# Optimization experiments

Hardware: AMD Instinct MI355X
Metric: run time of the kernel (lower is better)

## Reference

```python
import jax, jax.numpy as jnp
import numpy as np

N_NODES = 100000
N_EDGES = 1600000
IN_DIM = 128
HID = 64
OUT_DIM = 3


def _glorot(key, shape):
    fan_in, fan_out = shape[0], shape[1]
    std = (2.0 / (fan_in + fan_out)) ** 0.5
    return jax.random.normal(key, shape, jnp.float32) * std


def setup_inputs() -> dict:
    key = jax.random.key(0)
    ks = jax.random.split(key, 12)
    x = jax.random.normal(ks[0], (N_NODES, IN_DIM), jnp.float32)
    edge_index = jax.random.randint(ks[1], (2, N_EDGES), 0, N_NODES, dtype=jnp.int32)
    return {
        "x": x,
        "edge_index": edge_index,
        "W1": _glorot(ks[2], (IN_DIM, HID)), "b1": jnp.zeros((HID,), jnp.float32),
        "W2": _glorot(ks[3], (HID, HID)), "b2": jnp.zeros((HID,), jnp.float32),
        "W3": _glorot(ks[4], (HID, HID)), "b3": jnp.zeros((HID,), jnp.float32),
        "W4": _glorot(ks[5], (HID, HID // 2)), "b4": jnp.zeros((HID // 2,), jnp.float32),
        "Wh": _glorot(ks[6], (HID // 2, OUT_DIM)), "bh": jnp.zeros((OUT_DIM,), jnp.float32),
    }


def reference(x, edge_index, W1, b1, W2, b2, W3, b3, W4, b4, Wh, bh):
    n = x.shape[0]
    self_loops = jnp.arange(n, dtype=edge_index.dtype)
    src = jnp.concatenate([edge_index[0], self_loops])  # message sources j
    dst = jnp.concatenate([edge_index[1], self_loops])  # aggregation targets i
    # symmetric GCN normalization with self-loops: deg over targets (unit edge weights)
    deg = jax.ops.segment_sum(jnp.ones_like(dst, jnp.float32), dst, num_segments=n)
    dinv = jnp.where(deg > 0, jax.lax.rsqrt(deg), 0.0)
    norm = dinv[src] * dinv[dst]  # [E+N]

    def gcn(h, W, b):
        h = h @ W  # transform first (PyG GCNConv order)
        agg = jax.ops.segment_sum(h[src] * norm[:, None], dst, num_segments=n)
        return agg + b

    h = jax.nn.relu(gcn(x, W1, b1))   # dropout is identity in eval mode
    h = jax.nn.relu(gcn(h, W2, b2))
    h = jax.nn.relu(gcn(h, W3, b3))
    h = jax.nn.relu(gcn(h, W4, b4))
    return h @ Wh + bh  # [N, 3]
```

## Files before the change

kernel.cpp:

```cpp
#include <hip/hip_runtime.h>
#include <hip/hip_bf16.h>
#include <hip/hip_fp16.h>
#include <cstdint>


#define MAXD 512
#define EB   8192
#define PADSLACK 2048

__device__ __forceinline__ void hist_body(const int* __restrict__ ei,
                                          int* __restrict__ histM, int E, int b) {
    __shared__ int hist[MAXD];
    const int tid = threadIdx.x;
    hist[tid] = 0; hist[tid + 256] = 0;
    __syncthreads();
    const int base = b * EB;
#pragma unroll 2
    for (int it = 0; it < EB / 256; it += 4) {
        int d[4]; bool ok[4];
#pragma unroll
        for (int u = 0; u < 4; ++u) {
            int e = base + (it + u) * 256 + tid;
            ok[u] = e < E;
            d[u] = ok[u] ? ei[E + e] : 0;
        }
#pragma unroll
        for (int u = 0; u < 4; ++u)
            if (ok[u]) atomicAdd(&hist[d[u] >> 8], 1);
    }
    __syncthreads();
    histM[(size_t)b * MAXD + tid] = hist[tid];
    histM[(size_t)b * MAXD + tid + 256] = hist[tid + 256];
}

__global__ __launch_bounds__(256) void scan_digits_k(int* __restrict__ histM,
                                                     int* __restrict__ totals,
                                                     int NBLK) {
    __shared__ int s[256];
    const int t = threadIdx.x, dg = blockIdx.x;
    int v = (t < NBLK) ? histM[(size_t)t * MAXD + dg] : 0;
    s[t] = v;
    __syncthreads();
    for (int off = 1; off < 256; off <<= 1) {
        int x = (t >= off) ? s[t - off] : 0;
        __syncthreads();
        s[t] += x;
        __syncthreads();
    }
    if (t < NBLK) histM[(size_t)t * MAXD + dg] = s[t] - v;
    if (t == 255) totals[dg] = s[255];
}

__global__ __launch_bounds__(512) void scan_base_k(const int* __restrict__ totals,
                                                   int* __restrict__ cb, int ND) {
    __shared__ int s[512];
    const int t = threadIdx.x;
    int v = (t < ND) ? totals[t] : 0;
    s[t] = v;
    __syncthreads();
    for (int off = 1; off < 512; off <<= 1) {
        int x = (t >= off) ? s[t - off] : 0;
        __syncthreads();
        s[t] += x;
        __syncthreads();
    }
    if (t < ND) cb[t] = s[t] - v;
    if (t == 511) cb[ND] = s[511];
}

template <int K, int OUT, bool HALF_OUT>
__device__ __forceinline__ void gemm_body(const float* __restrict__ H,
                                          const float* __restrict__ W,
                                          const float* __restrict__ dinv,
                                          void* __restrict__ Tout, int n, int bx) {
    constexpr int TX  = OUT / 4;
    constexpr int TY  = 256 / TX;
    constexpr int BM  = TY * 4;
    constexpr int BK  = 32;
    constexpr int PAD = 4;

    __shared__ float At[BK][BM + PAD];
    __shared__ float Ws[BK][OUT];

    const int t    = threadIdx.x;
    const int cx   = t % TX;
    const int ry   = t / TX;
    const int row0 = bx * BM;

    float acc[4][4] = {{0.f}};
    const int arow = t >> 3;
    const int af4  = t & 7;

    for (int k0 = 0; k0 < K; k0 += BK) {
#pragma unroll
        for (int p = 0; p < BM / 32; ++p) {
            int r  = arow + p * 32;
            int gr = row0 + r;
            int grc = gr < n ? gr : n - 1;
            float4 v = *reinterpret_cast<const float4*>(
                H + (size_t)grc * K + k0 + af4 * 4);
            At[af4 * 4 + 0][r] = v.x;
            At[af4 * 4 + 1][r] = v.y;
            At[af4 * 4 + 2][r] = v.z;
            At[af4 * 4 + 3][r] = v.w;
        }
#pragma unroll
        for (int p = 0; p < (BK * OUT) / 1024; ++p) {
            int idx = t + p * 256;
            int wk  = idx / (OUT / 4);
            int wf  = idx % (OUT / 4);
            float4 v = *reinterpret_cast<const float4*>(
                W + (size_t)(k0 + wk) * OUT + wf * 4);
            *reinterpret_cast<float4*>(&Ws[wk][wf * 4]) = v;
        }
        __syncthreads();
#pragma unroll
        for (int k = 0; k < BK; ++k) {
            float4 a = *reinterpret_cast<const float4*>(&At[k][ry * 4]);
            float4 w = *reinterpret_cast<const float4*>(&Ws[k][cx * 4]);
            acc[0][0] = fmaf(a.x, w.x, acc[0][0]);
            acc[0][1] = fmaf(a.x, w.y, acc[0][1]);
            acc[0][2] = fmaf(a.x, w.z, acc[0][2]);
            acc[0][3] = fmaf(a.x, w.w, acc[0][3]);
            acc[1][0] = fmaf(a.y, w.x, acc[1][0]);
            acc[1][1] = fmaf(a.y, w.y, acc[1][1]);
            acc[1][2] = fmaf(a.y, w.z, acc[1][2]);
            acc[1][3] = fmaf(a.y, w.w, acc[1][3]);
            acc[2][0] = fmaf(a.z, w.x, acc[2][0]);
            acc[2][1] = fmaf(a.z, w.y, acc[2][1]);
            acc[2][2] = fmaf(a.z, w.z, acc[2][2]);
            acc[2][3] = fmaf(a.z, w.w, acc[2][3]);
            acc[3][0] = fmaf(a.w, w.x, acc[3][0]);
            acc[3][1] = fmaf(a.w, w.y, acc[3][1]);
            acc[3][2] = fmaf(a.w, w.z, acc[3][2]);
            acc[3][3] = fmaf(a.w, w.w, acc[3][3]);
        }
        __syncthreads();
    }
#pragma unroll
    for (int i = 0; i < 4; ++i) {
        int gr = row0 + ry * 4 + i;
        if (gr < n) {
            if constexpr (HALF_OUT) {
                float di = dinv[gr];
                union { ushort4 u; __half h[4]; } pk;
                pk.h[0] = __float2half_rn(acc[i][0] * di);
                pk.h[1] = __float2half_rn(acc[i][1] * di);
                pk.h[2] = __float2half_rn(acc[i][2] * di);
                pk.h[3] = __float2half_rn(acc[i][3] * di);
                *reinterpret_cast<ushort4*>(
                    (__half*)Tout + (size_t)gr * 64 + cx * 4) = pk.u;
            } else {
                float4 v = make_float4(acc[i][0], acc[i][1], acc[i][2], acc[i][3]);
                *reinterpret_cast<float4*>(
                    (float*)Tout + (size_t)gr * OUT + cx * 4) = v;
            }
        }
    }
}

__device__ __forceinline__ void pack_body(const int* __restrict__ ei,
                                          const int* __restrict__ histM,
                                          const int* __restrict__ cb,
                                          int* __restrict__ packed,
                                          int E, int ND, int b) {
    __shared__ int cur[MAXD];
    const int tid = threadIdx.x;
    for (int t = tid; t < ND; t += 256)
        cur[t] = cb[t] + histM[(size_t)b * MAXD + t];
    __syncthreads();
    const int base = b * EB;
    for (int it = 0; it < EB / 256; it += 4) {
        int s[4], d[4]; bool ok[4];
#pragma unroll
        for (int u = 0; u < 4; ++u) {
            int e = base + (it + u) * 256 + tid;
            ok[u] = e < E;
            if (ok[u]) { s[u] = ei[e]; d[u] = ei[E + e]; }
        }
#pragma unroll
        for (int u = 0; u < 4; ++u) {
            if (ok[u]) {
                int pos = atomicAdd(&cur[d[u] >> 8], 1);
                packed[pos] = (s[u] << 8) | (d[u] & 255);
            }
        }
    }
}

__global__ __launch_bounds__(256) void hist_gemm1_k(
    const int* __restrict__ ei, int* __restrict__ histM, int E,
    const float* __restrict__ x, const float* __restrict__ W1,
    float* __restrict__ T1, int n, int NH) {
    const int bx = blockIdx.x;
    if (bx < NH) hist_body(ei, histM, E, bx);
    else         gemm_body<128, 64, false>(x, W1, nullptr, T1, n, bx - NH);
}

__global__ __launch_bounds__(256) void pack_gemm1_k(
    const int* __restrict__ ei, const int* __restrict__ histM,
    const int* __restrict__ cb, int* __restrict__ packed,
    const float* __restrict__ x, const float* __restrict__ W1,
    float* __restrict__ T1, int n, int E, int ND, int NPB, int G1) {
    const int bx = blockIdx.x;
    if (bx < NPB) pack_body(ei, histM, cb, packed, E, ND, bx);
    else          gemm_body<128, 64, false>(x, W1, nullptr, T1, n, G1 + bx - NPB);
}

__global__ __launch_bounds__(256) void bucket_k(const int* __restrict__ packed,
                                                const int* __restrict__ cb,
                                                int* __restrict__ col,
                                                int* __restrict__ rowptr,
                                                int* __restrict__ counts,
                                                float* __restrict__ dinv,
                                                const float* __restrict__ Traw,
                                                __half* __restrict__ Th, int n) {
    __shared__ int   hist[256];
    __shared__ int   pref[256];
    __shared__ int   cur[256];
    __shared__ float dinv_l[256];

    const int tid   = threadIdx.x;
    const int dg    = blockIdx.x;
    const int base  = cb[dg];
    const int m     = cb[dg + 1] - base;
    const int basep = base + dg * PADSLACK;

    hist[tid] = 0;
    __syncthreads();
    for (int k0 = 0; k0 < m; k0 += 1024) {
        int v[4]; bool ok[4];
#pragma unroll
        for (int u = 0; u < 4; ++u) {
            int k = k0 + u * 256 + tid;
            ok[u] = k < m;
            v[u] = ok[u] ? packed[base + k] : 0;
        }
#pragma unroll
        for (int u = 0; u < 4; ++u)
            if (ok[u]) atomicAdd(&hist[v[u] & 255], 1);
    }
    __syncthreads();
    const int deg   = hist[tid];
    const int cnt_p = (deg + 8) & ~7;
    pref[tid] = cnt_p;
    __syncthreads();
    for (int off = 1; off < 256; off <<= 1) {
        int x = (tid >= off) ? pref[tid - off] : 0;
        __syncthreads();
        pref[tid] += x;
        __syncthreads();
    }
    const int rp = basep + pref[tid] - cnt_p;
    const float di = rsqrtf((float)(deg + 1));
    dinv_l[tid] = di;
    cur[tid] = rp + 1;
    const int d = dg * 256 + tid;
    if (d < n) {
        counts[d] = cnt_p;
        dinv[d]   = di;
        rowptr[d] = rp;
        col[rp]   = d;
        for (int k = deg + 1; k < cnt_p; ++k) col[rp + k] = n;
    }
    __syncthreads();
    for (int k0 = 0; k0 < m; k0 += 1024) {
        int v[4]; bool ok[4];
#pragma unroll
        for (int u = 0; u < 4; ++u) {
            int k = k0 + u * 256 + tid;
            ok[u] = k < m;
            v[u] = ok[u] ? packed[base + k] : 0;
        }
#pragma unroll
        for (int u = 0; u < 4; ++u) {
            if (ok[u]) {
                int pos = atomicAdd(&cur[v[u] & 255], 1);
                col[pos] = v[u] >> 8;
            }
        }
    }
    const int r0 = dg * 256;
#pragma unroll 4
    for (int it = 0; it < 16; ++it) {
        int idx = it * 256 + tid;
        int rl  = idx >> 4;
        int r   = r0 + rl;
        if (r < n) {
            float4 v = reinterpret_cast<const float4*>(Traw)[(size_t)r * 16 + (idx & 15)];
            float dd = dinv_l[rl];
            union { ushort4 u; __half h[4]; } pk;
            pk.h[0] = __float2half_rn(v.x * dd);
            pk.h[1] = __float2half_rn(v.y * dd);
            pk.h[2] = __float2half_rn(v.z * dd);
            pk.h[3] = __float2half_rn(v.w * dd);
            reinterpret_cast<ushort4*>(Th)[(size_t)r * 16 + (idx & 15)] = pk.u;
        }
    }
    if (dg == 0 && tid < 16) {
        uint2 z; z.x = 0u; z.y = 0u;
        reinterpret_cast<uint2*>(Th)[(size_t)n * 16 + tid] = z;
    }
}

template <int K, int OUT>
__global__ __launch_bounds__(256) void gemm_h_k(const float* __restrict__ H,
                                                const float* __restrict__ W,
                                                const float* __restrict__ dinv,
                                                __half* __restrict__ T, int n) {
    gemm_body<K, OUT, true>(H, W, dinv, T, n, blockIdx.x);
}

template <int LR, bool FUSE_HEAD>
__global__ __launch_bounds__(256) void agg_k(const __half* __restrict__ T,
                                             const int* __restrict__ rowptr,
                                             const int* __restrict__ counts,
                                             const int* __restrict__ col,
                                             const float* __restrict__ dinv,
                                             const float* __restrict__ bias,
                                             float* __restrict__ O, int n,
                                             const float* __restrict__ Wh,
                                             const float* __restrict__ bh) {
    constexpr int NSW = 64 / LR;
    constexpr int U   = 16 / NSW;
    constexpr int UH  = U / 2;
    const int lane = threadIdx.x & 63;
    const int q    = lane % LR;
    const int sw   = lane / LR;
    const int i = (blockIdx.x * blockDim.x + threadIdx.x) >> 6;
    if (i >= n) return;

    const int start = rowptr[i];
    const int cnt   = counts[i];
    const uint2* __restrict__ T2 = reinterpret_cast<const uint2*>(T);

    float4 acc = make_float4(0.f, 0.f, 0.f, 0.f);
    for (int base = 0; base < cnt; base += 64) {
        const int m = min(64, cnt - base);
        int c_l = col[start + base + lane];
        int jg = 0;
        for (; jg + 16 <= m; jg += 16) {
            int cc[U]; uint2 v[U];
#pragma unroll
            for (int u = 0; u < U; ++u)
                cc[u] = __shfl(c_l, jg + u * NSW + sw, 64);
#pragma unroll
            for (int u = 0; u < U; ++u) v[u] = T2[(size_t)cc[u] * 16 + q];
#pragma unroll
            for (int u = 0; u < U; ++u) {
                const __half2* h2 = reinterpret_cast<const __half2*>(&v[u]);
                float2 f0 = __half22float2(h2[0]);
                float2 f1 = __half22float2(h2[1]);
                acc.x += f0.x; acc.y += f0.y; acc.z += f1.x; acc.w += f1.y;
            }
        }
        if (jg < m) {
            int cc[UH]; uint2 v[UH];
#pragma unroll
            for (int u = 0; u < UH; ++u)
                cc[u] = __shfl(c_l, jg + u * NSW + sw, 64);
#pragma unroll
            for (int u = 0; u < UH; ++u) v[u] = T2[(size_t)cc[u] * 16 + q];
#pragma unroll
            for (int u = 0; u < UH; ++u) {
                const __half2* h2 = reinterpret_cast<const __half2*>(&v[u]);
                float2 f0 = __half22float2(h2[0]);
                float2 f1 = __half22float2(h2[1]);
                acc.x += f0.x; acc.y += f0.y; acc.z += f1.x; acc.w += f1.y;
            }
        }
    }
#pragma unroll
    for (int off = LR; off < 64; off <<= 1) {
        acc.x += __shfl_xor(acc.x, off, 64);
        acc.y += __shfl_xor(acc.y, off, 64);
        acc.z += __shfl_xor(acc.z, off, 64);
        acc.w += __shfl_xor(acc.w, off, 64);
    }
    const float di = dinv[i];
    const float4 b4 = reinterpret_cast<const float4*>(bias)[q];
    float4 h;
    h.x = fmaxf(fmaf(di, acc.x, b4.x), 0.f);
    h.y = fmaxf(fmaf(di, acc.y, b4.y), 0.f);
    h.z = fmaxf(fmaf(di, acc.z, b4.z), 0.f);
    h.w = fmaxf(fmaf(di, acc.w, b4.w), 0.f);
    if constexpr (!FUSE_HEAD) {
        if (sw == 0)
            reinterpret_cast<float4*>(O + (size_t)i * 64)[q] = h;
    } else {
        float p0 = h.x * Wh[(4 * q + 0) * 3 + 0];
        float p1 = h.x * Wh[(4 * q + 0) * 3 + 1];
        float p2 = h.x * Wh[(4 * q + 0) * 3 + 2];
        p0 = fmaf(h.y, Wh[(4 * q + 1) * 3 + 0], p0);
        p1 = fmaf(h.y, Wh[(4 * q + 1) * 3 + 1], p1);
        p2 = fmaf(h.y, Wh[(4 * q + 1) * 3 + 2], p2);
        p0 = fmaf(h.z, Wh[(4 * q + 2) * 3 + 0], p0);
        p1 = fmaf(h.z, Wh[(4 * q + 2) * 3 + 1], p1);
        p2 = fmaf(h.z, Wh[(4 * q + 2) * 3 + 2], p2);
        p0 = fmaf(h.w, Wh[(4 * q + 3) * 3 + 0], p0);
        p1 = fmaf(h.w, Wh[(4 * q + 3) * 3 + 1], p1);
        p2 = fmaf(h.w, Wh[(4 * q + 3) * 3 + 2], p2);
#pragma unroll
        for (int off = 1; off < LR; off <<= 1) {
            p0 += __shfl_xor(p0, off, 64);
            p1 += __shfl_xor(p1, off, 64);
            p2 += __shfl_xor(p2, off, 64);
        }
        if (lane == 0) {
            O[(size_t)i * 3 + 0] = p0 + bh[0];
            O[(size_t)i * 3 + 1] = p1 + bh[1];
            O[(size_t)i * 3 + 2] = p2 + bh[2];
        }
    }
}

extern "C" void kernel_launch(void* const* d_in, const int* in_sizes, int n_in,
                              void* d_out, int out_size, void* d_ws, size_t ws_size,
                              hipStream_t stream) {
    const float* x  = (const float*)d_in[0];
    const int*   ei = (const int*)d_in[1];
    const float* W1 = (const float*)d_in[2];
    const float* b1 = (const float*)d_in[3];
    const float* W2 = (const float*)d_in[4];
    const float* b2 = (const float*)d_in[5];
    const float* W3 = (const float*)d_in[6];
    const float* b3 = (const float*)d_in[7];
    const float* W4 = (const float*)d_in[8];
    const float* b4 = (const float*)d_in[9];
    const float* Wh = (const float*)d_in[10];
    const float* bh = (const float*)d_in[11];
    float* out = (float*)d_out;

    const int n = in_sizes[0] / 128;
    const int E = in_sizes[1] / 2;
    const int ND   = (n + 255) / 256;
    const int NBLK = (E + EB - 1) / EB;

    char* ws = (char*)d_ws;
    auto alloc = [&](size_t bytes) {
        char* p = ws;
        ws += (bytes + 255) & ~(size_t)255;
        return p;
    };
    int*    histM  = (int*)alloc((size_t)NBLK * MAXD * 4);
    int*    totals = (int*)alloc((size_t)MAXD * 4);
    int*    cbA    = (int*)alloc((size_t)(MAXD + 1) * 4);
    int*    packed = (int*)alloc((size_t)E * 4);
    int*    col    = (int*)alloc(((size_t)E + (size_t)ND * PADSLACK + 256) * 4);
    int*    rowptr = (int*)alloc((size_t)n * 4);
    int*    counts = (int*)alloc((size_t)n * 4);
    float*  dinv   = (float*)alloc((size_t)n * 4);
    float*  bufF   = (float*)alloc((size_t)n * 64 * 4);
    __half* bufH   = (__half*)alloc(((size_t)n + 1) * 64 * 2);

    dim3 blk(256);
    const int G  = (n + 63) / 64;
    const int G1 = G / 3;
    const int G2 = G - G1;
    const int agg_blocks = (n + 3) / 4;

    hist_gemm1_k<<<dim3(NBLK + G1), blk, 0, stream>>>(ei, histM, E, x, W1, bufF, n, NBLK);
    scan_digits_k<<<dim3(ND), blk, 0, stream>>>(histM, totals, NBLK);
    scan_base_k<<<dim3(1), dim3(512), 0, stream>>>(totals, cbA, ND);
    pack_gemm1_k<<<dim3(NBLK + G2), blk, 0, stream>>>(ei, histM, cbA, packed,
                                                      x, W1, bufF, n, E, ND, NBLK, G1);
    bucket_k<<<dim3(ND), blk, 0, stream>>>(packed, cbA, col, rowptr, counts,
                                           dinv, bufF, bufH, n);
    agg_k<16, false><<<dim3(agg_blocks), blk, 0, stream>>>(
        bufH, rowptr, counts, col, dinv, b1, bufF, n, nullptr, nullptr);
    gemm_h_k<64, 64><<<dim3(G), blk, 0, stream>>>(bufF, W2, dinv, bufH, n);
    agg_k<16, false><<<dim3(agg_blocks), blk, 0, stream>>>(
        bufH, rowptr, counts, col, dinv, b2, bufF, n, nullptr, nullptr);
    gemm_h_k<64, 64><<<dim3(G), blk, 0, stream>>>(bufF, W3, dinv, bufH, n);
    agg_k<16, false><<<dim3(agg_blocks), blk, 0, stream>>>(
        bufH, rowptr, counts, col, dinv, b3, bufF, n, nullptr, nullptr);
    gemm_h_k<64, 32><<<dim3((n + 127) / 128), blk, 0, stream>>>(bufF, W4, dinv, bufH, n);
    agg_k<8, true><<<dim3(agg_blocks), blk, 0, stream>>>(
        bufH, rowptr, counts, col, dinv, b4, out, n, Wh, bh);
}
```

Baseline: 383.9 us.

## Use fp16 MFMA for hidden GEMMs and store aggregation outputs in fp16

```diff
diff --git a/kernel.cpp b/kernel.cpp
--- a/kernel.cpp
+++ b/kernel.cpp
@@ -7,6 +7,24 @@
 #define MAXD 512
 #define EB   8192
 #define PADSLACK 2048
+
+typedef _Float16 half8v __attribute__((ext_vector_type(8)));
+typedef _Float16 half2v __attribute__((ext_vector_type(2)));
+typedef float    float4v __attribute__((ext_vector_type(4)));
+
+#if defined(__has_builtin)
+#if __has_builtin(__builtin_amdgcn_fdot2)
+#define HAVE_FDOT2 1
+#endif
+#endif
+
+__device__ __forceinline__ float fdot2f(half2v a, half2v b, float c) {
+#ifdef HAVE_FDOT2
+    return __builtin_amdgcn_fdot2(a, b, c, false);
+#else
+    return c + (float)a[0] * (float)b[0] + (float)a[1] * (float)b[1];
+#endif
+}
 
 __device__ __forceinline__ void hist_body(const int* __restrict__ ei,
                                           int* __restrict__ histM, int E, int b) {
@@ -68,11 +86,10 @@
     if (t == 511) cb[ND] = s[511];
 }
 
-template <int K, int OUT, bool HALF_OUT>
+template <int K, int OUT>
 __device__ __forceinline__ void gemm_body(const float* __restrict__ H,
                                           const float* __restrict__ W,
-                                          const float* __restrict__ dinv,
-                                          void* __restrict__ Tout, int n, int bx) {
+                                          float* __restrict__ Tout, int n, int bx) {
     constexpr int TX  = OUT / 4;
     constexpr int TY  = 256 / TX;
     constexpr int BM  = TY * 4;
@@ -141,20 +158,8 @@
     for (int i = 0; i < 4; ++i) {
         int gr = row0 + ry * 4 + i;
         if (gr < n) {
-            if constexpr (HALF_OUT) {
-                float di = dinv[gr];
-                union { ushort4 u; __half h[4]; } pk;
-                pk.h[0] = __float2half_rn(acc[i][0] * di);
-                pk.h[1] = __float2half_rn(acc[i][1] * di);
-                pk.h[2] = __float2half_rn(acc[i][2] * di);
-                pk.h[3] = __float2half_rn(acc[i][3] * di);
-                *reinterpret_cast<ushort4*>(
-                    (__half*)Tout + (size_t)gr * 64 + cx * 4) = pk.u;
-            } else {
-                float4 v = make_float4(acc[i][0], acc[i][1], acc[i][2], acc[i][3]);
-                *reinterpret_cast<float4*>(
-                    (float*)Tout + (size_t)gr * OUT + cx * 4) = v;
-            }
+            float4 v = make_float4(acc[i][0], acc[i][1], acc[i][2], acc[i][3]);
+            *reinterpret_cast<float4*>(Tout + (size_t)gr * OUT + cx * 4) = v;
         }
     }
 }
@@ -194,7 +199,7 @@
     float* __restrict__ T1, int n, int NH) {
     const int bx = blockIdx.x;
     if (bx < NH) hist_body(ei, histM, E, bx);
-    else         gemm_body<128, 64, false>(x, W1, nullptr, T1, n, bx - NH);
+    else         gemm_body<128, 64>(x, W1, T1, n, bx - NH);
 }
 
 __global__ __launch_bounds__(256) void pack_gemm1_k(
@@ -204,7 +209,7 @@
     float* __restrict__ T1, int n, int E, int ND, int NPB, int G1) {
     const int bx = blockIdx.x;
     if (bx < NPB) pack_body(ei, histM, cb, packed, E, ND, bx);
-    else          gemm_body<128, 64, false>(x, W1, nullptr, T1, n, G1 + bx - NPB);
+    else          gemm_body<128, 64>(x, W1, T1, n, G1 + bx - NPB);
 }
 
 __global__ __launch_bounds__(256) void bucket_k(const int* __restrict__ packed,
@@ -303,12 +308,55 @@
     }
 }
 
-template <int K, int OUT>
-__global__ __launch_bounds__(256) void gemm_h_k(const float* __restrict__ H,
-                                                const float* __restrict__ W,
-                                                const float* __restrict__ dinv,
-                                                __half* __restrict__ T, int n) {
-    gemm_body<K, OUT, true>(H, W, dinv, T, n, blockIdx.x);
+template <int OUT>
+__global__ __launch_bounds__(256) void gemm_mfma_k(
+    const _Float16* __restrict__ H, const float* __restrict__ W,
+    const float* __restrict__ dinv, _Float16* __restrict__ T, int n) {
+    constexpr int NT = OUT / 16;
+    const int lane = threadIdx.x & 63;
+    const int m16  = lane & 15;
+    const int quad = lane >> 4;
+    const int wid  = (blockIdx.x * blockDim.x + threadIdx.x) >> 6;
+    const int nw   = (gridDim.x * blockDim.x) >> 6;
+
+    half8v bfrag[NT][2];
+#pragma unroll
+    for (int t = 0; t < NT; ++t)
+#pragma unroll
+        for (int h = 0; h < 2; ++h)
+#pragma unroll
+            for (int j = 0; j < 8; ++j)
+                bfrag[t][h][j] = (_Float16)W[(size_t)(h * 32 + quad * 8 + j) * OUT
+                                             + t * 16 + m16];
+
+    const int nblk = (n + 15) >> 4;
+    for (int rb = wid; rb < nblk; rb += nw) {
+        const int r0 = rb * 16;
+        int ra = r0 + m16; if (ra >= n) ra = n - 1;
+        const half8v* hrow = reinterpret_cast<const half8v*>(H + (size_t)ra * 64);
+        half8v a0 = hrow[quad];
+        half8v a1 = hrow[4 + quad];
+
+        float4v dfr[NT];
+#pragma unroll
+        for (int t = 0; t < NT; ++t) {
+            float4v z = {0.f, 0.f, 0.f, 0.f};
+            z = __builtin_amdgcn_mfma_f32_16x16x32_f16(a0, bfrag[t][0], z, 0, 0, 0);
+            z = __builtin_amdgcn_mfma_f32_16x16x32_f16(a1, bfrag[t][1], z, 0, 0, 0);
+            dfr[t] = z;
+        }
+#pragma unroll
+        for (int reg = 0; reg < 4; ++reg) {
+            int row = r0 + quad * 4 + reg;
+            if (row < n) {
+                float di = dinv[row];
+#pragma unroll
+                for (int t = 0; t < NT; ++t)
+                    T[(size_t)row * 64 + t * 16 + m16] =
+                        (_Float16)(dfr[t][reg] * di);
+            }
+        }
+    }
 }
 
 template <int LR, bool FUSE_HEAD>
@@ -318,7 +366,7 @@
                                              const int* __restrict__ col,
                                              const float* __restrict__ dinv,
                                              const float* __restrict__ bias,
-                                             float* __restrict__ O, int n,
+                                             void* __restrict__ O, int n,
                                              const float* __restrict__ Wh,
                                              const float* __restrict__ bh) {
     constexpr int NSW = 64 / LR;
@@ -330,6 +378,9 @@
     const int i = (blockIdx.x * blockDim.x + threadIdx.x) >> 6;
     if (i >= n) return;
 
+    const half2v s10 = {(_Float16)1.f, (_Float16)0.f};
+    const half2v s01 = {(_Float16)0.f, (_Float16)1.f};
+
     const int start = rowptr[i];
     const int cnt   = counts[i];
     const uint2* __restrict__ T2 = reinterpret_cast<const uint2*>(T);
@@ -348,10 +399,11 @@
             for (int u = 0; u < U; ++u) v[u] = T2[(size_t)cc[u] * 16 + q];
 #pragma unroll
             for (int u = 0; u < U; ++u) {
-                const __half2* h2 = reinterpret_cast<const __half2*>(&v[u]);
-                float2 f0 = __half22float2(h2[0]);
-                float2 f1 = __half22float2(h2[1]);
-                acc.x += f0.x; acc.y += f0.y; acc.z += f1.x; acc.w += f1.y;
+                union { uint2 uu; half2v h[2]; } cv; cv.uu = v[u];
+                acc.x = fdot2f(cv.h[0], s10, acc.x);
+                acc.y = fdot2f(cv.h[0], s01, acc.y);
+                acc.z = fdot2f(cv.h[1], s10, acc.z);
+                acc.w = fdot2f(cv.h[1], s01, acc.w);
             }
         }
         if (jg < m) {
@@ -363,10 +415,11 @@
             for (int u = 0; u < UH; ++u) v[u] = T2[(size_t)cc[u] * 16 + q];
 #pragma unroll
             for (int u = 0; u < UH; ++u) {
-                const __half2* h2 = reinterpret_cast<const __half2*>(&v[u]);
-                float2 f0 = __half22float2(h2[0]);
-                float2 f1 = __half22float2(h2[1]);
-                acc.x += f0.x; acc.y += f0.y; acc.z += f1.x; acc.w += f1.y;
+                union { uint2 uu; half2v h[2]; } cv; cv.uu = v[u];
+                acc.x = fdot2f(cv.h[0], s10, acc.x);
+                acc.y = fdot2f(cv.h[0], s01, acc.y);
+                acc.z = fdot2f(cv.h[1], s10, acc.z);
+                acc.w = fdot2f(cv.h[1], s01, acc.w);
             }
         }
     }
@@ -385,9 +438,17 @@
     h.z = fmaxf(fmaf(di, acc.z, b4.z), 0.f);
     h.w = fmaxf(fmaf(di, acc.w, b4.w), 0.f);
     if constexpr (!FUSE_HEAD) {
-        if (sw == 0)
-            reinterpret_cast<float4*>(O + (size_t)i * 64)[q] = h;
+        if (sw == 0) {
+            union { ushort4 u; __half hh[4]; } pk;
+            pk.hh[0] = __float2half_rn(h.x);
+            pk.hh[1] = __float2half_rn(h.y);
+            pk.hh[2] = __float2half_rn(h.z);
+            pk.hh[3] = __float2half_rn(h.w);
+            ushort* base_p = (ushort*)O + (size_t)i * 64;
+            *reinterpret_cast<ushort4*>(base_p + 4 * q) = pk.u;
+        }
     } else {
+        float* Of = (float*)O;
         float p0 = h.x * Wh[(4 * q + 0) * 3 + 0];
         float p1 = h.x * Wh[(4 * q + 0) * 3 + 1];
         float p2 = h.x * Wh[(4 * q + 0) * 3 + 2];
@@ -407,9 +468,9 @@
             p2 += __shfl_xor(p2, off, 64);
         }
         if (lane == 0) {
-            O[(size_t)i * 3 + 0] = p0 + bh[0];
-            O[(size_t)i * 3 + 1] = p1 + bh[1];
-            O[(size_t)i * 3 + 2] = p2 + bh[2];
+            Of[(size_t)i * 3 + 0] = p0 + bh[0];
+            Of[(size_t)i * 3 + 1] = p1 + bh[1];
+            Of[(size_t)i * 3 + 2] = p2 + bh[2];
         }
     }
 }
@@ -452,12 +513,14 @@
     float*  dinv   = (float*)alloc((size_t)n * 4);
     float*  bufF   = (float*)alloc((size_t)n * 64 * 4);
     __half* bufH   = (__half*)alloc(((size_t)n + 1) * 64 * 2);
+    __half* bufG   = (__half*)bufF;
 
     dim3 blk(256);
     const int G  = (n + 63) / 64;
     const int G1 = G / 3;
     const int G2 = G - G1;
     const int agg_blocks = (n + 3) / 4;
+    const int mfma_blocks = 640;
 
     hist_gemm1_k<<<dim3(NBLK + G1), blk, 0, stream>>>(ei, histM, E, x, W1, bufF, n, NBLK);
     scan_digits_k<<<dim3(ND), blk, 0, stream>>>(histM, totals, NBLK);
@@ -467,14 +530,17 @@
     bucket_k<<<dim3(ND), blk, 0, stream>>>(packed, cbA, col, rowptr, counts,
                                            dinv, bufF, bufH, n);
     agg_k<16, false><<<dim3(agg_blocks), blk, 0, stream>>>(
-        bufH, rowptr, counts, col, dinv, b1, bufF, n, nullptr, nullptr);
-    gemm_h_k<64, 64><<<dim3(G), blk, 0, stream>>>(bufF, W2, dinv, bufH, n);
+        bufH, rowptr, counts, col, dinv, b1, bufG, n, nullptr, nullptr);
+    gemm_mfma_k<64><<<dim3(mfma_blocks), blk, 0, stream>>>(
+        (const _Float16*)bufG, W2, dinv, (_Float16*)bufH, n);
     agg_k<16, false><<<dim3(agg_blocks), blk, 0, stream>>>(
-        bufH, rowptr, counts, col, dinv, b2, bufF, n, nullptr, nullptr);
-    gemm_h_k<64, 64><<<dim3(G), blk, 0, stream>>>(bufF, W3, dinv, bufH, n);
+        bufH, rowptr, counts, col, dinv, b2, bufG, n, nullptr, nullptr);
+    gemm_mfma_k<64><<<dim3(mfma_blocks), blk, 0, stream>>>(
+        (const _Float16*)bufG, W3, dinv, (_Float16*)bufH, n);
     agg_k<16, false><<<dim3(agg_blocks), blk, 0, stream>>>(
-        bufH, rowptr, counts, col, dinv, b3, bufF, n, nullptr, nullptr);
-    gemm_h_k<64, 32><<<dim3((n + 127) / 128), blk, 0, stream>>>(bufF, W4, dinv, bufH, n);
+        bufH, rowptr, counts, col, dinv, b3, bufG, n, nullptr, nullptr);
+    gemm_mfma_k<32><<<dim3(mfma_blocks), blk, 0, stream>>>(
+        (const _Float16*)bufG, W4, dinv, (_Float16*)bufH, n);
     agg_k<8, true><<<dim3(agg_blocks), blk, 0, stream>>>(
         bufH, rowptr, counts, col, dinv, b4, out, n, Wh, bh);
 }
```

After: 365.7 us. -4.7%, faster.
